# Kernel optimization log

Measured on AMD Instinct MI355X. Metric: run time of the kernel, lower is better.

Reference implementation:

```python
import jax, jax.numpy as jnp
import numpy as np
from jax import lax

WIN = 7  # hard-coded winsize in PSF.forward
EPS = 1e-8


def _box_sum(x, n):
    # Sliding n x n window sum with zero padding (== ZeroPad2d(n//2) + unfold sum),
    return lax.reduce_window(x, 0.0, lax.add, (1, 1, n, n), (1, 1, 1, 1), 'SAME')


def _patch_stats(x, n):
    n2 = n * n
    s = _box_sum(x, n)
    s2 = _box_sum(x * x, n)
    mean = s / n2
    # torch .var() default is unbiased (divide by N-1)
    var = (s2 - n2 * mean * mean) / (n2 - 1)
    return mean, jnp.maximum(var, 0.0)


def patch_mv_norm(x, n):
    mean, var = _patch_stats(x, n)
    return (x - mean) / (jnp.sqrt(var) + EPS)


def patch_adain(x, y, n):
    x_norm = patch_mv_norm(x, n)
    y_mean, y_var = _patch_stats(y, n)
    return x_norm * jnp.sqrt(y_var) + y_mean  # note: no eps on y_std, as in source


def conv1x1(x, w, b):
    # x: (B,C,H,W), w: (O,C), b: (O,)
    return jnp.einsum('oc,bchw->bohw', w, x) + b[None, :, None, None]


def setup_inputs() -> dict:
    key = jax.random.key(0)
    ks = jax.random.split(key, 12)
    B, C, H, W = 8, 256, 128, 128
    front = jax.random.normal(ks[0], (B, C, H, W), dtype=jnp.float32)
    back = jax.random.normal(ks[1], (B, C, H, W), dtype=jnp.float32)
    mask = jax.random.uniform(ks[2], (B, 1, H, W), dtype=jnp.float32)
    scale = 0.02
    we = jax.random.normal(ks[3], (C, C), dtype=jnp.float32) * scale
    wf = jax.random.normal(ks[4], (C, C), dtype=jnp.float32) * scale
    wg = jax.random.normal(ks[5], (C, C), dtype=jnp.float32) * scale
    wh = jax.random.normal(ks[6], (C, C), dtype=jnp.float32) * scale
    be = jax.random.normal(ks[7], (C,), dtype=jnp.float32) * scale
    bf = jax.random.normal(ks[8], (C,), dtype=jnp.float32) * scale
    bg = jax.random.normal(ks[9], (C,), dtype=jnp.float32) * scale
    bh = jax.random.normal(ks[10], (C,), dtype=jnp.float32) * scale
    return {'front': front, 'back': back, 'mask': mask,
            'we': we, 'be': be, 'wf': wf, 'bf': bf,
            'wg': wg, 'bg': bg, 'wh': wh, 'bh': bh}


def reference(front, back, mask, we, be, wf, bf, wg, bg, wh, bh):
    b, c, h, w = front.shape
    EE = conv1x1(patch_adain(front, back, WIN), we, be)
    FF = conv1x1(patch_mv_norm(front, WIN), wf, bf)
    GG = conv1x1(patch_mv_norm(back, WIN), wg, bg)
    HH = conv1x1(back, wh, bh)
    # channel-wise cosine similarity between FF and GG
    F_n = jnp.sqrt(jnp.sum(FF * FF, axis=1))  # (B,H,W)
    G_n = jnp.sqrt(jnp.sum(GG * GG, axis=1))
    S = jnp.sum(FF * GG, axis=1) / (F_n * G_n)
    # per-sample spatial min-max normalization
    S_flat = S.reshape(b, h * w)
    s_min = jnp.min(S_flat, axis=1, keepdims=True)
    s_max = jnp.max(S_flat, axis=1, keepdims=True)
    S_n = ((S_flat - s_min) / (s_max - s_min)).reshape(b, 1, h, w)
    fused = S_n * EE + (1.0 - S_n) * HH
    return fused
```

## Files before the change

kernel.cpp:

```cpp
#include <hip/hip_runtime.h>
#include <math.h>

#define PIX 16384
#define TSZ ((size_t)33554432)

typedef __attribute__((ext_vector_type(8))) short  short8;
typedef __attribute__((ext_vector_type(4))) float  float4v;
typedef __attribute__((ext_vector_type(4))) unsigned int uint4v;
typedef __attribute__((ext_vector_type(2))) unsigned int uint2v;

__device__ __forceinline__ unsigned short f2bf(float x) {
  unsigned int u = __float_as_uint(x);
  u += 0x7fffu + ((u >> 16) & 1u);
  return (unsigned short)(u >> 16);
}
__device__ __forceinline__ float bf2f(unsigned short h) {
  return __uint_as_float(((unsigned int)h) << 16);
}
__device__ __forceinline__ unsigned int pack_bf2(float lo, float hi) {
  unsigned int ul = __float_as_uint(lo); ul += 0x7fffu + ((ul >> 16) & 1u);
  unsigned int uh = __float_as_uint(hi); uh += 0x7fffu + ((uh >> 16) & 1u);
  return __builtin_amdgcn_perm(uh, ul, 0x07060302u);
}

__global__ __launch_bounds__(256) void k_prep(const float* __restrict__ we,
                                              const float* __restrict__ wf,
                                              const float* __restrict__ wg,
                                              const float* __restrict__ wh,
                                              unsigned short* __restrict__ wbf) {
  int idx = blockIdx.x * 256 + threadIdx.x;
  int g = idx >> 16, within = idx & 65535;
  const float* src = (g == 0) ? wf : (g == 1) ? wg : (g == 2) ? we : wh;
  int e    = within & 7;
  int lane = (within >> 3) & 63;
  int im   = (within >> 9) & 3;
  int wv   = (within >> 11) & 3;
  int i    = within >> 13;
  int col = lane & 15, q = lane >> 4;
  int m = wv * 64 + im * 16 + col;
  int k = i * 32 + q * 8 + e;
  wbf[idx] = f2bf(src[m * 256 + k]);
}

__global__ __launch_bounds__(256, 4) void k_stats(const float* __restrict__ front,
                                                  const float* __restrict__ back,
                                                  unsigned short* __restrict__ xcm) {
  int blk = blockIdx.x;
  int s   = blk & 7;
  int c   = (blk >> 3) & 255;
  int b   = blk >> 11;
  int t   = threadIdx.x;
  int r0  = s * 16;

  __shared__ float  xs[22 * 129];
  __shared__ float2 vsp[16 * 131];
  __shared__ unsigned long long obI[16 * 64];

  size_t planeOff = ((size_t)(b * 256 + c)) * PIX;

  float meanR[8], sdR[8];

  #pragma unroll 1
  for (int phase = 0; phase < 2; ++phase) {
    const float* src = (phase == 0 ? back : front) + planeOff;
    #pragma unroll
    for (int i = 0; i < 3; ++i) {
      int idx = t + i * 256;
      if (idx < 704) {
        int l = idx >> 5, cv = (idx & 31) * 4;
        int g = r0 - 3 + l;
        float4v v = {0.f, 0.f, 0.f, 0.f};
        if (g >= 0 && g < 128) v = *(const float4v*)(src + g * 128 + cv);
        xs[l * 129 + cv]     = v[0];
        xs[l * 129 + cv + 1] = v[1];
        xs[l * 129 + cv + 2] = v[2];
        xs[l * 129 + cv + 3] = v[3];
      }
    }
    __syncthreads();
    {
      int col = t & 127;
      int rg  = (t >> 7) * 8;
      float sm = 0.f, s2 = 0.f;
      #pragma unroll
      for (int j = 0; j < 7; ++j) { float v = xs[(rg + j) * 129 + col]; sm += v; s2 = fmaf(v, v, s2); }
      vsp[rg * 131 + col] = make_float2(sm, s2);
      #pragma unroll
      for (int o = 1; o < 8; ++o) {
        float vn = xs[(rg + o + 6) * 129 + col];
        float vo = xs[(rg + o - 1) * 129 + col];
        sm += vn - vo;
        s2 += vn * vn - vo * vo;
        vsp[(rg + o) * 131 + col] = make_float2(sm, s2);
      }
    }
    __syncthreads();
    {
      int r  = t & 15;
      int c0 = (t >> 4) * 8;
      float2 w[14];
      #pragma unroll
      for (int i = 0; i < 14; ++i) {
        int cc = c0 - 3 + i;
        float2 v = make_float2(0.f, 0.f);
        if (cc >= 0 && cc < 128) v = vsp[r * 131 + cc];
        w[i] = v;
      }
      float sm = 0.f, s2 = 0.f;
      #pragma unroll
      for (int i = 0; i < 7; ++i) { sm += w[i].x; s2 += w[i].y; }
      float nrmv[8], xv[8];
      #pragma unroll
      for (int o = 0; o < 8; ++o) {
        float mean = sm * (1.f / 49.f);
        float var  = (s2 - sm * mean) * (1.f / 48.f);
        var = var > 0.f ? var : 0.f;
        float sd = __builtin_amdgcn_sqrtf(var);
        float x  = xs[(r + 3) * 129 + c0 + o];
        float nrm = (x - mean) * __builtin_amdgcn_rcpf(sd + 1e-8f);
        if (phase == 0) { meanR[o] = mean; sdR[o] = sd; }
        nrmv[o] = nrm; xv[o] = x;
        if (o < 7) { sm += w[o + 7].x - w[o].x; s2 += w[o + 7].y - w[o].y; }
      }
      #pragma unroll
      for (int op = 0; op < 4; ++op) {
        unsigned int lo32 = pack_bf2(nrmv[2 * op], nrmv[2 * op + 1]);
        float h0, h1;
        if (phase == 0) { h0 = xv[2 * op]; h1 = xv[2 * op + 1]; }
        else {
          h0 = nrmv[2 * op]     * sdR[2 * op]     + meanR[2 * op];
          h1 = nrmv[2 * op + 1] * sdR[2 * op + 1] + meanR[2 * op + 1];
        }
        unsigned int hi32 = pack_bf2(h0, h1);
        int m = (c0 >> 1) + op;
        obI[r * 64 + ((m + r) & 63)] = ((unsigned long long)hi32 << 32) | lo32;
      }
    }
    __syncthreads();
    {
      int r  = t >> 4;
      int mg = (t & 15) * 4;
      unsigned int t0[4], t1[4];
      #pragma unroll
      for (int k2 = 0; k2 < 4; ++k2) {
        unsigned long long v = obI[r * 64 + ((mg + k2 + r) & 63)];
        t0[k2] = (unsigned int)v;
        t1[k2] = (unsigned int)(v >> 32);
      }
      int p = (r0 + r) * 128 + mg * 2;
      size_t gb2 = (((size_t)(b * 256 + (p >> 6))) * 256 + c) * 64 + (p & 63);
      int tn0 = (phase == 0) ? 1 : 0;
      int tn1 = (phase == 0) ? 3 : 2;
      *(uint4v*)(xcm + (size_t)tn0 * TSZ + gb2) = (uint4v){t0[0], t0[1], t0[2], t0[3]};
      *(uint4v*)(xcm + (size_t)tn1 * TSZ + gb2) = (uint4v){t1[0], t1[1], t1[2], t1[3]};
    }
  }
}

#define SB0   __builtin_amdgcn_sched_barrier(0)
#define BARR  __builtin_amdgcn_s_barrier()
#define LGKM0 asm volatile("s_waitcnt lgkmcnt(0)" ::: "memory")
#define VMC(n) asm volatile("s_waitcnt vmcnt(" #n ")" ::: "memory")

__device__ __forceinline__ void stage_tile(const unsigned short* __restrict__ Xt,
                                           int k0, int t,
                                           unsigned short* dst) {
  int kk = ((t >> 5) << 2) + ((t & 7) >> 1);
  int px = (((t >> 3) & 3) << 4) + ((t & 1) << 3);
  const unsigned short* src = Xt + (size_t)(k0 << 6) + (kk << 6) + px;
  typedef const __attribute__((address_space(1))) unsigned int GUI;
  typedef __attribute__((address_space(3))) unsigned int LUI;
  __builtin_amdgcn_global_load_lds((GUI*)(unsigned long long)src,
                                   (LUI*)(unsigned)(unsigned long long)(dst + t * 8),
                                   16, 0, 0);
}

#define LOADA(S, I) {                                           \
  af[S][0] = *(const short8*)(Wr + (I) * 8192 + 0 * 512);       \
  af[S][1] = *(const short8*)(Wr + (I) * 8192 + 1 * 512);       \
  af[S][2] = *(const short8*)(Wr + (I) * 8192 + 2 * 512);       \
  af[S][3] = *(const short8*)(Wr + (I) * 8192 + 3 * 512); }

#define TR8(O0,O1,O2,O3,O4,O5,O6,O7)                                              \
  asm volatile("ds_read_b64_tr_b16 %0, %1 offset:" #O0 : "=v"(r0) : "v"(tra));    \
  asm volatile("ds_read_b64_tr_b16 %0, %1 offset:" #O1 : "=v"(r1) : "v"(tra));    \
  asm volatile("ds_read_b64_tr_b16 %0, %1 offset:" #O2 : "=v"(r2) : "v"(tra));    \
  asm volatile("ds_read_b64_tr_b16 %0, %1 offset:" #O3 : "=v"(r3) : "v"(tra));    \
  asm volatile("ds_read_b64_tr_b16 %0, %1 offset:" #O4 : "=v"(r4) : "v"(tra));    \
  asm volatile("ds_read_b64_tr_b16 %0, %1 offset:" #O5 : "=v"(r5) : "v"(tra));    \
  asm volatile("ds_read_b64_tr_b16 %0, %1 offset:" #O6 : "=v"(r6) : "v"(tra));    \
  asm volatile("ds_read_b64_tr_b16 %0, %1 offset:" #O7 : "=v"(r7) : "v"(tra));

#define DOMFMA(MS) {                                                        \
  union BU { unsigned u[4]; short8 s; } bu0, bu1, bu2, bu3;                 \
  bu0.u[0]=r0[0]; bu0.u[1]=r0[1]; bu0.u[2]=r1[0]; bu0.u[3]=r1[1];           \
  bu1.u[0]=r2[0]; bu1.u[1]=r2[1]; bu1.u[2]=r3[0]; bu1.u[3]=r3[1];           \
  bu2.u[0]=r4[0]; bu2.u[1]=r4[1]; bu2.u[2]=r5[0]; bu2.u[3]=r5[1];           \
  bu3.u[0]=r6[0]; bu3.u[1]=r6[1]; bu3.u[2]=r7[0]; bu3.u[3]=r7[1];           \
  short8 bv0 = bu0.s, bv1 = bu1.s, bv2 = bu2.s, bv3 = bu3.s;                \
  _Pragma("unroll")                                                         \
  for (int im = 0; im < 4; ++im) {                                          \
    acc[0][im] = __builtin_amdgcn_mfma_f32_16x16x32_bf16(af[MS][im], bv0, acc[0][im], 0, 0, 0); \
    acc[1][im] = __builtin_amdgcn_mfma_f32_16x16x32_bf16(af[MS][im], bv1, acc[1][im], 0, 0, 0); \
    acc[2][im] = __builtin_amdgcn_mfma_f32_16x16x32_bf16(af[MS][im], bv2, acc[2][im], 0, 0, 0); \
    acc[3][im] = __builtin_amdgcn_mfma_f32_16x16x32_bf16(af[MS][im], bv3, acc[3][im], 0, 0, 0); \
  } }

#define GSTEP(VN, DOSTAGE, K0, SLOT, DOA, AS, AI, MS, O0,O1,O2,O3,O4,O5,O6,O7) \
  SB0;                                                                          \
  if (DOSTAGE) stage_tile(X, K0, t, xt + (SLOT) * 2048);                        \
  SB0;                                                                          \
  if (DOA) LOADA(AS, AI);                                                       \
  SB0;                                                                          \
  VMC(VN);                                                                      \
  SB0; BARR; SB0;                                                               \
  TR8(O0,O1,O2,O3,O4,O5,O6,O7);                                                 \
  LGKM0; SB0;                                                                   \
  DOMFMA(MS);

__device__ __forceinline__ void gemm_pipe(const unsigned short* __restrict__ X,
                                          const unsigned short* __restrict__ Wm,
                                          unsigned short* xt, unsigned xbase,
                                          int mbase, int lane, int t,
                                          float4v acc[4][4]) {
  unsigned tra = xbase + (unsigned)((((lane >> 4)) << 10) + ((lane & 15) << 3));
  const unsigned short* __restrict__ Wr = Wm + ((mbase >> 6) << 11) + lane * 8;

  short8 af[3][4];
  uint2v r0, r1, r2, r3, r4, r5, r6, r7;

  #pragma unroll
  for (int in = 0; in < 4; ++in)
    #pragma unroll
    for (int im = 0; im < 4; ++im)
      acc[in][im] = (float4v){0.f, 0.f, 0.f, 0.f};

  SB0; BARR; SB0;
  stage_tile(X,  0, t, xt + 0 * 2048);
  stage_tile(X, 32, t, xt + 1 * 2048);
  stage_tile(X, 64, t, xt + 2 * 2048);
  SB0;
  LOADA(0, 0);
  SB0;
  LOADA(1, 1);
  SB0;

  GSTEP( 9,  1,  96,  3,   1, 2, 2, 0,      0,  512,  128,  640,  256,  768,  384,  896)
  GSTEP(10,  1, 128,  4,   1, 0, 3, 1,   4096, 4608, 4224, 4736, 4352, 4864, 4480, 4992)
  GSTEP(10,  1, 160,  0,   1, 1, 4, 2,   8192, 8704, 8320, 8832, 8448, 8960, 8576, 9088)
  GSTEP(10,  1, 192,  1,   1, 2, 5, 0,  12288,12800,12416,12928,12544,13056,12672,13184)
  GSTEP(10,  1, 224,  2,   1, 0, 6, 1,  16384,16896,16512,17024,16640,17152,16768,17280)
  GSTEP( 9,  0,   0,  0,   1, 1, 7, 2,      0,  512,  128,  640,  256,  768,  384,  896)
  GSTEP( 4,  0,   0,  0,   0, 0, 0, 0,   4096, 4608, 4224, 4736, 4352, 4864, 4480, 4992)
  GSTEP( 0,  0,   0,  0,   0, 0, 0, 1,   8192, 8704, 8320, 8832, 8448, 8960, 8576, 9088)
}

__global__ __launch_bounds__(256, 2) void k_gemm(const unsigned short* __restrict__ xcm,
                                                 const unsigned short* __restrict__ wbf,
                                                 const float* __restrict__ bFF,
                                                 const float* __restrict__ bGG,
                                                 const float* __restrict__ bEE,
                                                 const float* __restrict__ bHH,
                                                 unsigned short* __restrict__ eecm,
                                                 unsigned short* __restrict__ hhcm,
                                                 float* __restrict__ Sout) {
  int blk  = blockIdx.x;
  int b    = blk >> 8;
  int pt   = blk & 255;
  int p0   = pt * 64;
  int t    = threadIdx.x;
  int wv   = t >> 6;
  int lane = t & 63;
  int col  = lane & 15;
  int q    = lane >> 4;
  int mbase = wv * 64;

  __shared__ __align__(16) unsigned short xt[5][2048];
  __shared__ float sred[3 * 64];
  if (t < 192) sred[t] = 0.f;
  __syncthreads();
  unsigned xbase = (unsigned)(unsigned long long)&xt[0][0];

  const unsigned short* Xt = xcm + (((size_t)(b * 256 + pt)) << 14);

  float4v aF[4][4], aG[4][4];

  gemm_pipe(Xt + 0 * TSZ, wbf + 0 * 65536, &xt[0][0], xbase, mbase, lane, t, aF);
  gemm_pipe(Xt + 1 * TSZ, wbf + 1 * 65536, &xt[0][0], xbase, mbase, lane, t, aG);
  #pragma unroll
  for (int im = 0; im < 4; ++im) {
    float4v bvF = *(const float4v*)(bFF + mbase + im * 16 + q * 4);
    float4v bvG = *(const float4v*)(bGG + mbase + im * 16 + q * 4);
    #pragma unroll
    for (int in = 0; in < 4; ++in) { aF[in][im] += bvF; aG[in][im] += bvG; }
  }
  #pragma unroll
  for (int in = 0; in < 4; ++in) {
    float d = 0.f, nf = 0.f, ng = 0.f;
    #pragma unroll
    for (int im = 0; im < 4; ++im)
      #pragma unroll
      for (int r = 0; r < 4; ++r) {
        float f = aF[in][im][r], g = aG[in][im][r];
        d += f * g; nf += f * f; ng += g * g;
      }
    d  += __shfl_xor(d, 16);  d  += __shfl_xor(d, 32);
    nf += __shfl_xor(nf, 16); nf += __shfl_xor(nf, 32);
    ng += __shfl_xor(ng, 16); ng += __shfl_xor(ng, 32);
    if (lane < 16) {
      atomicAdd(&sred[0 * 64 + in * 16 + lane], d);
      atomicAdd(&sred[1 * 64 + in * 16 + lane], nf);
      atomicAdd(&sred[2 * 64 + in * 16 + lane], ng);
    }
  }
  gemm_pipe(Xt + 2 * TSZ, wbf + 2 * 65536, &xt[0][0], xbase, mbase, lane, t, aF);
  #pragma unroll
  for (int im = 0; im < 4; ++im) {
    float4v bv = *(const float4v*)(bEE + mbase + im * 16 + q * 4);
    #pragma unroll
    for (int in = 0; in < 4; ++in)
      #pragma unroll
      for (int r = 0; r < 4; ++r) {
        int m = mbase + im * 16 + q * 4 + r;
        eecm[((size_t)(b * 256 + m)) * PIX + p0 + in * 16 + col] = f2bf(aF[in][im][r] + bv[r]);
      }
  }
  gemm_pipe(Xt + 3 * TSZ, wbf + 3 * 65536, &xt[0][0], xbase, mbase, lane, t, aG);
  #pragma unroll
  for (int im = 0; im < 4; ++im) {
    float4v bv = *(const float4v*)(bHH + mbase + im * 16 + q * 4);
    #pragma unroll
    for (int in = 0; in < 4; ++in)
      #pragma unroll
      for (int r = 0; r < 4; ++r) {
        int m = mbase + im * 16 + q * 4 + r;
        hhcm[((size_t)(b * 256 + m)) * PIX + p0 + in * 16 + col] = f2bf(aG[in][im][r] + bv[r]);
      }
  }
  __syncthreads();
  if (t < 64) {
    float d = sred[t], nf = sred[64 + t], ng = sred[128 + t];
    Sout[(size_t)b * PIX + p0 + t] = d / (sqrtf(nf) * sqrtf(ng));
  }
}

__global__ __launch_bounds__(256) void k_minmax(const float* __restrict__ S,
                                                float* __restrict__ mm) {
  int b = blockIdx.x, t = threadIdx.x;
  const float* sp = S + (size_t)b * PIX;
  float mn = 3.0e38f, mx = -3.0e38f;
  for (int i = t; i < PIX; i += 256) { float v = sp[i]; mn = fminf(mn, v); mx = fmaxf(mx, v); }
  #pragma unroll
  for (int o = 32; o >= 1; o >>= 1) {
    mn = fminf(mn, __shfl_xor(mn, o));
    mx = fmaxf(mx, __shfl_xor(mx, o));
  }
  __shared__ float smn[4], smx[4];
  if ((t & 63) == 0) { smn[t >> 6] = mn; smx[t >> 6] = mx; }
  __syncthreads();
  if (t == 0) {
    mn = fminf(fminf(smn[0], smn[1]), fminf(smn[2], smn[3]));
    mx = fmaxf(fmaxf(smx[0], smx[1]), fmaxf(smx[2], smx[3]));
    mm[b * 2] = mn; mm[b * 2 + 1] = mx;
  }
}

__global__ __launch_bounds__(256) void k_blend(const unsigned short* __restrict__ ee,
                                               const unsigned short* __restrict__ hh,
                                               const float* __restrict__ S,
                                               const float* __restrict__ mm,
                                               float* __restrict__ out) {
  size_t base = ((size_t)blockIdx.x * 256 + threadIdx.x) * 4;
  int b = (int)(base >> 22);
  int p = (int)(base & 16383);
  float mn = mm[b * 2], mx = mm[b * 2 + 1];
  float inv = 1.f / (mx - mn);
  uint2v eu = *(const uint2v*)(ee + base);
  uint2v hu = *(const uint2v*)(hh + base);
  float4v s0 = *(const float4v*)(S + ((size_t)b << 14) + p);
  float ov[4];
  #pragma unroll
  for (int i = 0; i < 2; ++i) {
    unsigned int ew = eu[i], hw = hu[i];
    float e0 = bf2f((unsigned short)(ew & 0xffffu));
    float e1 = bf2f((unsigned short)(ew >> 16));
    float h0 = bf2f((unsigned short)(hw & 0xffffu));
    float h1 = bf2f((unsigned short)(hw >> 16));
    float a0 = (s0[2 * i] - mn) * inv;
    float a1 = (s0[2 * i + 1] - mn) * inv;
    ov[2 * i]     = h0 + a0 * (e0 - h0);
    ov[2 * i + 1] = h1 + a1 * (e1 - h1);
  }
  *(float4v*)(out + base) = (float4v){ov[0], ov[1], ov[2], ov[3]};
}

extern "C" void kernel_launch(void* const* d_in, const int* in_sizes, int n_in,
                              void* d_out, int out_size, void* d_ws, size_t ws_size,
                              hipStream_t stream) {
  const float* front = (const float*)d_in[0];
  const float* back  = (const float*)d_in[1];
  const float* we = (const float*)d_in[3];
  const float* be = (const float*)d_in[4];
  const float* wf = (const float*)d_in[5];
  const float* bf = (const float*)d_in[6];
  const float* wg = (const float*)d_in[7];
  const float* bg = (const float*)d_in[8];
  const float* wh = (const float*)d_in[9];
  const float* bh = (const float*)d_in[10];

  char* ws = (char*)d_ws;
  unsigned short* xcm  = (unsigned short*)(ws);
  unsigned short* wbf  = (unsigned short*)(ws + 268435456);
  unsigned short* eecm = (unsigned short*)(ws + 268959744);
  unsigned short* hhcm = (unsigned short*)(ws + 336068608);
  float*          S    = (float*)(ws + 403177472);
  float*          mm   = (float*)(ws + 403701760);
  float*          out  = (float*)d_out;

  k_prep  <<<1024,  256, 0, stream>>>(we, wf, wg, wh, wbf);
  k_stats <<<16384, 256, 0, stream>>>(front, back, xcm);
  k_gemm  <<<2048,  256, 0, stream>>>(xcm, wbf, bf, bg, be, bh, eecm, hhcm, S);
  k_minmax<<<8,     256, 0, stream>>>(S, mm);
  k_blend <<<32768, 256, 0, stream>>>(eecm, hhcm, S, mm, out);
}
```

Measured before the change: 593.3 us.

## Split GEMM into similarity and output passes, fusing blend into second GEMM

The single GEMM kernel is split in two. The first computes only the FF/GG projections and the cosine similarity S. The second runs after the min-max reduction, computes the EE/HH projections, and writes the blended fp32 output directly. This removes the bf16 EE/HH intermediate round trip (write plus re-read) and the separate blend kernel, at the cost of an extra kernel launch and re-reading the staged input for the second pass. EE and HH are now kept in fp32 rather than rounded to bf16 before blending.

```diff
diff --git a/kernel.cpp b/kernel.cpp
--- a/kernel.cpp
+++ b/kernel.cpp
@@ -255,15 +255,73 @@
   GSTEP( 0,  0,   0,  0,   0, 0, 0, 1,   8192, 8704, 8320, 8832, 8448, 8960, 8576, 9088)
 }
 
-__global__ __launch_bounds__(256, 2) void k_gemm(const unsigned short* __restrict__ xcm,
-                                                 const unsigned short* __restrict__ wbf,
-                                                 const float* __restrict__ bFF,
-                                                 const float* __restrict__ bGG,
-                                                 const float* __restrict__ bEE,
-                                                 const float* __restrict__ bHH,
-                                                 unsigned short* __restrict__ eecm,
-                                                 unsigned short* __restrict__ hhcm,
-                                                 float* __restrict__ Sout) {
+__global__ __launch_bounds__(256, 2) void k_gemm1(const unsigned short* __restrict__ xcm,
+                                                  const unsigned short* __restrict__ wbf,
+                                                  const float* __restrict__ bFF,
+                                                  const float* __restrict__ bGG,
+                                                  float* __restrict__ Sout) {
+  int blk  = blockIdx.x;
+  int b    = blk >> 8;
+  int pt   = blk & 255;
+  int p0   = pt * 64;
+  int t    = threadIdx.x;
+  int wv   = t >> 6;
+  int lane = t & 63;
+  int q    = lane >> 4;
+  int mbase = wv * 64;
+
+  __shared__ __align__(16) unsigned short xt[5][2048];
+  __shared__ float sred[3 * 64];
+  if (t < 192) sred[t] = 0.f;
+  __syncthreads();
+  unsigned xbase = (unsigned)(unsigned long long)&xt[0][0];
+
+  const unsigned short* Xt = xcm + (((size_t)(b * 256 + pt)) << 14);
+
+  float4v aF[4][4], aG[4][4];
+
+  gemm_pipe(Xt + 0 * TSZ, wbf + 0 * 65536, &xt[0][0], xbase, mbase, lane, t, aF);
+  gemm_pipe(Xt + 1 * TSZ, wbf + 1 * 65536, &xt[0][0], xbase, mbase, lane, t, aG);
+  #pragma unroll
+  for (int im = 0; im < 4; ++im) {
+    float4v bvF = *(const float4v*)(bFF + mbase + im * 16 + q * 4);
+    float4v bvG = *(const float4v*)(bGG + mbase + im * 16 + q * 4);
+    #pragma unroll
+    for (int in = 0; in < 4; ++in) { aF[in][im] += bvF; aG[in][im] += bvG; }
+  }
+  #pragma unroll
+  for (int in = 0; in < 4; ++in) {
+    float d = 0.f, nf = 0.f, ng = 0.f;
+    #pragma unroll
+    for (int im = 0; im < 4; ++im)
+      #pragma unroll
+      for (int r = 0; r < 4; ++r) {
+        float f = aF[in][im][r], g = aG[in][im][r];
+        d += f * g; nf += f * f; ng += g * g;
+      }
+    d  += __shfl_xor(d, 16);  d  += __shfl_xor(d, 32);
+    nf += __shfl_xor(nf, 16); nf += __shfl_xor(nf, 32);
+    ng += __shfl_xor(ng, 16); ng += __shfl_xor(ng, 32);
+    if (lane < 16) {
+      atomicAdd(&sred[0 * 64 + in * 16 + lane], d);
+      atomicAdd(&sred[1 * 64 + in * 16 + lane], nf);
+      atomicAdd(&sred[2 * 64 + in * 16 + lane], ng);
+    }
+  }
+  __syncthreads();
+  if (t < 64) {
+    float d = sred[t], nf = sred[64 + t], ng = sred[128 + t];
+    Sout[(size_t)b * PIX + p0 + t] = d / (sqrtf(nf) * sqrtf(ng));
+  }
+}
+
+__global__ __launch_bounds__(256, 2) void k_gemm2(const unsigned short* __restrict__ xcm,
+                                                  const unsigned short* __restrict__ wbf,
+                                                  const float* __restrict__ bEE,
+                                                  const float* __restrict__ bHH,
+                                                  const float* __restrict__ S,
+                                                  const float* __restrict__ mm,
+                                                  float* __restrict__ out) {
   int blk  = blockIdx.x;
   int b    = blk >> 8;
   int pt   = blk & 255;
@@ -276,71 +334,35 @@
   int mbase = wv * 64;
 
   __shared__ __align__(16) unsigned short xt[5][2048];
-  __shared__ float sred[3 * 64];
-  if (t < 192) sred[t] = 0.f;
-  __syncthreads();
   unsigned xbase = (unsigned)(unsigned long long)&xt[0][0];
 
   const unsigned short* Xt = xcm + (((size_t)(b * 256 + pt)) << 14);
 
-  float4v aF[4][4], aG[4][4];
-
-  gemm_pipe(Xt + 0 * TSZ, wbf + 0 * 65536, &xt[0][0], xbase, mbase, lane, t, aF);
-  gemm_pipe(Xt + 1 * TSZ, wbf + 1 * 65536, &xt[0][0], xbase, mbase, lane, t, aG);
+  float4v aE[4][4], aH[4][4];
+
+  gemm_pipe(Xt + 2 * TSZ, wbf + 2 * 65536, &xt[0][0], xbase, mbase, lane, t, aE);
+  gemm_pipe(Xt + 3 * TSZ, wbf + 3 * 65536, &xt[0][0], xbase, mbase, lane, t, aH);
+
+  float mn = mm[b * 2], mx = mm[b * 2 + 1];
+  float inv = 1.f / (mx - mn);
+  float sn[4];
+  #pragma unroll
+  for (int in = 0; in < 4; ++in)
+    sn[in] = (S[(size_t)b * PIX + p0 + in * 16 + col] - mn) * inv;
+
   #pragma unroll
   for (int im = 0; im < 4; ++im) {
-    float4v bvF = *(const float4v*)(bFF + mbase + im * 16 + q * 4);
-    float4v bvG = *(const float4v*)(bGG + mbase + im * 16 + q * 4);
-    #pragma unroll
-    for (int in = 0; in < 4; ++in) { aF[in][im] += bvF; aG[in][im] += bvG; }
-  }
-  #pragma unroll
-  for (int in = 0; in < 4; ++in) {
-    float d = 0.f, nf = 0.f, ng = 0.f;
-    #pragma unroll
-    for (int im = 0; im < 4; ++im)
-      #pragma unroll
-      for (int r = 0; r < 4; ++r) {
-        float f = aF[in][im][r], g = aG[in][im][r];
-        d += f * g; nf += f * f; ng += g * g;
-      }
-    d  += __shfl_xor(d, 16);  d  += __shfl_xor(d, 32);
-    nf += __shfl_xor(nf, 16); nf += __shfl_xor(nf, 32);
-    ng += __shfl_xor(ng, 16); ng += __shfl_xor(ng, 32);
-    if (lane < 16) {
-      atomicAdd(&sred[0 * 64 + in * 16 + lane], d);
-      atomicAdd(&sred[1 * 64 + in * 16 + lane], nf);
-      atomicAdd(&sred[2 * 64 + in * 16 + lane], ng);
-    }
-  }
-  gemm_pipe(Xt + 2 * TSZ, wbf + 2 * 65536, &xt[0][0], xbase, mbase, lane, t, aF);
-  #pragma unroll
-  for (int im = 0; im < 4; ++im) {
-    float4v bv = *(const float4v*)(bEE + mbase + im * 16 + q * 4);
+    float4v bvE = *(const float4v*)(bEE + mbase + im * 16 + q * 4);
+    float4v bvH = *(const float4v*)(bHH + mbase + im * 16 + q * 4);
     #pragma unroll
     for (int in = 0; in < 4; ++in)
       #pragma unroll
       for (int r = 0; r < 4; ++r) {
         int m = mbase + im * 16 + q * 4 + r;
-        eecm[((size_t)(b * 256 + m)) * PIX + p0 + in * 16 + col] = f2bf(aF[in][im][r] + bv[r]);
-      }
-  }
-  gemm_pipe(Xt + 3 * TSZ, wbf + 3 * 65536, &xt[0][0], xbase, mbase, lane, t, aG);
-  #pragma unroll
-  for (int im = 0; im < 4; ++im) {
-    float4v bv = *(const float4v*)(bHH + mbase + im * 16 + q * 4);
-    #pragma unroll
-    for (int in = 0; in < 4; ++in)
-      #pragma unroll
-      for (int r = 0; r < 4; ++r) {
-        int m = mbase + im * 16 + q * 4 + r;
-        hhcm[((size_t)(b * 256 + m)) * PIX + p0 + in * 16 + col] = f2bf(aG[in][im][r] + bv[r]);
-      }
-  }
-  __syncthreads();
-  if (t < 64) {
-    float d = sred[t], nf = sred[64 + t], ng = sred[128 + t];
-    Sout[(size_t)b * PIX + p0 + t] = d / (sqrtf(nf) * sqrtf(ng));
+        float e = aE[in][im][r] + bvE[r];
+        float h = aH[in][im][r] + bvH[r];
+        out[((size_t)(b * 256 + m)) * PIX + p0 + in * 16 + col] = h + sn[in] * (e - h);
+      }
   }
 }
 
@@ -363,35 +385,6 @@
     mx = fmaxf(fmaxf(smx[0], smx[1]), fmaxf(smx[2], smx[3]));
     mm[b * 2] = mn; mm[b * 2 + 1] = mx;
   }
-}
-
-__global__ __launch_bounds__(256) void k_blend(const unsigned short* __restrict__ ee,
-                                               const unsigned short* __restrict__ hh,
-                                               const float* __restrict__ S,
-                                               const float* __restrict__ mm,
-                                               float* __restrict__ out) {
-  size_t base = ((size_t)blockIdx.x * 256 + threadIdx.x) * 4;
-  int b = (int)(base >> 22);
-  int p = (int)(base & 16383);
-  float mn = mm[b * 2], mx = mm[b * 2 + 1];
-  float inv = 1.f / (mx - mn);
-  uint2v eu = *(const uint2v*)(ee + base);
-  uint2v hu = *(const uint2v*)(hh + base);
-  float4v s0 = *(const float4v*)(S + ((size_t)b << 14) + p);
-  float ov[4];
-  #pragma unroll
-  for (int i = 0; i < 2; ++i) {
-    unsigned int ew = eu[i], hw = hu[i];
-    float e0 = bf2f((unsigned short)(ew & 0xffffu));
-    float e1 = bf2f((unsigned short)(ew >> 16));
-    float h0 = bf2f((unsigned short)(hw & 0xffffu));
-    float h1 = bf2f((unsigned short)(hw >> 16));
-    float a0 = (s0[2 * i] - mn) * inv;
-    float a1 = (s0[2 * i + 1] - mn) * inv;
-    ov[2 * i]     = h0 + a0 * (e0 - h0);
-    ov[2 * i + 1] = h1 + a1 * (e1 - h1);
-  }
-  *(float4v*)(out + base) = (float4v){ov[0], ov[1], ov[2], ov[3]};
 }
 
 extern "C" void kernel_launch(void* const* d_in, const int* in_sizes, int n_in,
@@ -411,15 +404,13 @@
   char* ws = (char*)d_ws;
   unsigned short* xcm  = (unsigned short*)(ws);
   unsigned short* wbf  = (unsigned short*)(ws + 268435456);
-  unsigned short* eecm = (unsigned short*)(ws + 268959744);
-  unsigned short* hhcm = (unsigned short*)(ws + 336068608);
-  float*          S    = (float*)(ws + 403177472);
-  float*          mm   = (float*)(ws + 403701760);
+  float*          S    = (float*)(ws + 268959744);
+  float*          mm   = (float*)(ws + 269484032);
   float*          out  = (float*)d_out;
 
   k_prep  <<<1024,  256, 0, stream>>>(we, wf, wg, wh, wbf);
   k_stats <<<16384, 256, 0, stream>>>(front, back, xcm);
-  k_gemm  <<<2048,  256, 0, stream>>>(xcm, wbf, bf, bg, be, bh, eecm, hhcm, S);
+  k_gemm1 <<<2048,  256, 0, stream>>>(xcm, wbf, bf, bg, S);
   k_minmax<<<8,     256, 0, stream>>>(S, mm);
-  k_blend <<<32768, 256, 0, stream>>>(eecm, hhcm, S, mm, out);
-}
+  k_gemm2 <<<2048,  256, 0, stream>>>(xcm, wbf, be, bh, S, mm, out);
+}
```

After: 522.7 us. 11.9% less time.
